# Kernel optimization log

Measured on AMD Instinct MI355X. Metric: run time of the kernel, lower is better.

The kernel has to match this reference:

```python
import jax, jax.numpy as jnp
import numpy as np

B = 256       # number of grasp centers (batch)
N = 65536     # total points output by the backbone
C = 1024      # backbone feature channels (enc_channels[-1])
K = 512       # padded slots per segment (points per center)
INFO = 3      # info_size
KCLS = 6      # k_cls
EPS = 1e-5    # LayerNorm eps


def _layernorm(x, g, b):
    m = x.mean(-1, keepdims=True)
    v = ((x - m) ** 2).mean(-1, keepdims=True)
    return (x - m) / jnp.sqrt(v + EPS) * g + b


def setup_inputs() -> dict:
    key = jax.random.key(0)
    ks = jax.random.split(key, 10)
    feat = jax.random.normal(ks[0], (N, C), jnp.float32)
    offsets = jnp.sort(jax.random.randint(ks[1], (B,), 0, N)).astype(jnp.int64)
    offsets = offsets.at[-1].set(N)  # cumulative ends, last covers all points
    info = jax.random.normal(ks[2], (B, INFO), jnp.float32)

    def lin(k, o, i):
        return 0.02 * jax.random.normal(k, (o, i), jnp.float32), jnp.zeros((o,), jnp.float32)

    W1, b1 = lin(ks[3], 512, C)          # point_layer Linear(1024,512)
    Wi, bi = lin(ks[4], 32, INFO)        # info_layer Linear(info_size,32)
    Wa1, ba1 = lin(ks[5], 256, 544)      # anchor_mlp Linear(544,256)
    Wa2, ba2 = lin(ks[6], KCLS, 256)     # anchor_mlp Linear(256,k_cls)
    Wo1, bo1 = lin(ks[7], 256, 544)      # offset_mlp Linear(544,256)
    Wo2, bo2 = lin(ks[8], KCLS * 3, 256) # offset_mlp Linear(256,k_cls*3)
    return dict(
        feat=feat, info=info, offsets=offsets,
        W1=W1, b1=b1, ln1_g=jnp.ones((512,)), ln1_b=jnp.zeros((512,)),
        Wi=Wi, bi=bi,
        Wa1=Wa1, ba1=ba1, lna_g=jnp.ones((256,)), lna_b=jnp.zeros((256,)),
        Wa2=Wa2, ba2=ba2,
        Wo1=Wo1, bo1=bo1, lno_g=jnp.ones((256,)), lno_b=jnp.zeros((256,)),
        Wo2=Wo2, bo2=bo2,
    )


def reference(feat, info, W1, b1, ln1_g, ln1_b, Wi, bi,
              Wa1, ba1, lna_g, lna_b, Wa2, ba2,
              Wo1, bo1, lno_g, lno_b, Wo2, bo2, offsets):
    # --- fused segment-max replaces the pad loop + max over padded dim ---
    # point i belongs to segment b s.t. offsets[b-1] <= i < offsets[b]
    ids = jnp.searchsorted(offsets, jnp.arange(feat.shape[0]), side='right')
    segmax = jax.ops.segment_max(feat, ids, num_segments=B)  # (B, C)
    lengths = jnp.diff(offsets, prepend=0)
    # original zero-pads to K slots: segments shorter than K see 0 in the max
    features = jnp.where((lengths < K)[:, None], jnp.maximum(segmax, 0.0), segmax)

    # point_layer: Linear -> LayerNorm -> Dropout(eval: identity) -> ReLU
    pf = jax.nn.relu(_layernorm(features @ W1.T + b1, ln1_g, ln1_b))
    # info_layer
    inf = info @ Wi.T + bi
    x = jnp.concatenate([pf, inf], axis=1)  # (B, 544)

    pred = jax.nn.relu(_layernorm(x @ Wa1.T + ba1, lna_g, lna_b)) @ Wa2.T + ba2
    off = jax.nn.relu(_layernorm(x @ Wo1.T + bo1, lno_g, lno_b)) @ Wo2.T + bo2
    offset = off.reshape(-1, KCLS, 3)
    return features, pred, offset
```

## Files before the change

### kernel.cpp

```cpp
#include <hip/hip_runtime.h>
#include <hip/hip_bf16.h>
#include <cstdint>

#define NPTS 65536
#define CCH  1024
#define BSEG 256
#define KSLOT 512
#define WROWS 32

typedef float v4f __attribute__((ext_vector_type(4)));

__device__ __forceinline__ unsigned ukey(float f) {
  int i = __float_as_int(f);
  return i >= 0 ? ((unsigned)i | 0x80000000u) : ~(unsigned)i;
}
__device__ __forceinline__ float udec(unsigned u, bool rl) {
  float v;
  if (u >= 0x80000000u) v = __int_as_float((int)(u & 0x7FFFFFFFu));
  else                  v = __int_as_float((int)~u);
  if (u == 0u) v = -__builtin_inff();
  if (rl) v = fmaxf(v, 0.0f);
  return v;
}

__device__ __forceinline__ v4f ntload4(const float* p) {
  return __builtin_nontemporal_load((const v4f*)p);
}
__device__ __forceinline__ v4f vmax4(v4f a, v4f b) {
  v4f r;
  r.x = fmaxf(a.x, b.x); r.y = fmaxf(a.y, b.y);
  r.z = fmaxf(a.z, b.z); r.w = fmaxf(a.w, b.w);
  return r;
}

__global__ __launch_bounds__(256) void segmax_k(const float* __restrict__ feat,
                                                const int* __restrict__ offsets,
                                                unsigned* __restrict__ keys) {
  int t = threadIdx.x;
  int col = t << 2;
  int row0 = blockIdx.x * WROWS;
  int row_end = row0 + WROWS;
  int lo = 0, hi = BSEG - 1;
  while (lo < hi) { int mid = (lo + hi) >> 1; if (offsets[mid] > row0) hi = mid; else lo = mid + 1; }
  int seg = lo;
  int end = offsets[seg];
  const float NI = -__builtin_inff();
  v4f m; m.x = NI; m.y = NI; m.z = NI; m.w = NI;
  bool dirty = false;
  int r = row0;
  while (r < row_end) {
    while (r >= end) {
      if (dirty) {
        unsigned* kp = keys + (size_t)seg * CCH + col;
        atomicMax(kp + 0, ukey(m.x));
        atomicMax(kp + 1, ukey(m.y));
        atomicMax(kp + 2, ukey(m.z));
        atomicMax(kp + 3, ukey(m.w));
        m.x = NI; m.y = NI; m.z = NI; m.w = NI;
        dirty = false;
      }
      ++seg;
      end = offsets[seg];
    }
    int stop = min(row_end, end);
    const float* p = feat + (size_t)r * CCH + col;
    for (; r + 8 <= stop; r += 8) {
      v4f v0 = ntload4(p);
      v4f v1 = ntload4(p + CCH);
      v4f v2 = ntload4(p + 2 * CCH);
      v4f v3 = ntload4(p + 3 * CCH);
      v4f v4 = ntload4(p + 4 * CCH);
      v4f v5 = ntload4(p + 5 * CCH);
      v4f v6 = ntload4(p + 6 * CCH);
      v4f v7 = ntload4(p + 7 * CCH);
      p += 8 * CCH;
      m = vmax4(m, vmax4(vmax4(vmax4(v0, v1), vmax4(v2, v3)),
                         vmax4(vmax4(v4, v5), vmax4(v6, v7))));
    }
    for (; r < stop; ++r) {
      v4f v = ntload4(p);
      p += CCH;
      m = vmax4(m, v);
    }
    dirty = true;
  }
  if (dirty) {
    unsigned* kp = keys + (size_t)seg * CCH + col;
    atomicMax(kp + 0, ukey(m.x));
    atomicMax(kp + 1, ukey(m.y));
    atomicMax(kp + 2, ukey(m.z));
    atomicMax(kp + 3, ukey(m.w));
  }
}

__global__ __launch_bounds__(256) void gemm1_fused(
    const unsigned* __restrict__ keys, const int* __restrict__ offsets,
    const float* __restrict__ W1, float* __restrict__ features,
    float* __restrict__ part) {
  __shared__ float As[32][68];
  __shared__ float Ws[32][68];
  int bx = blockIdx.x, by = blockIdx.y, bz = blockIdx.z;
  int t = threadIdx.x;
  int tx = t & 15, ty = t >> 4;
  int lr = t >> 3;
  int lk = (t & 7) << 2;
  int row0 = by * 64 + lr, row1 = row0 + 32;
  int len0 = offsets[row0] - (row0 ? offsets[row0 - 1] : 0);
  int len1 = offsets[row1] - offsets[row1 - 1];
  bool rl0 = len0 < KSLOT, rl1 = len1 < KSLOT;
  const unsigned* K0 = keys + (size_t)row0 * CCH + lk;
  const unsigned* K1 = keys + (size_t)row1 * CCH + lk;
  int c0 = bx * 64 + lr, c1 = c0 + 32;
  const float* Wr0 = W1 + (size_t)c0 * CCH + lk;
  const float* Wr1 = W1 + (size_t)c1 * CCH + lk;
  float acc[4][4] = {};
  for (int s = 0; s < 8; ++s) {
    int k0 = (bz * 8 + s) << 5;
    uint4 ua = *(const uint4*)(K0 + k0);
    uint4 ub = *(const uint4*)(K1 + k0);
    float4 w0 = *(const float4*)(Wr0 + k0);
    float4 w1 = *(const float4*)(Wr1 + k0);
    float4 a0 = make_float4(udec(ua.x, rl0), udec(ua.y, rl0), udec(ua.z, rl0), udec(ua.w, rl0));
    float4 a1 = make_float4(udec(ub.x, rl1), udec(ub.y, rl1), udec(ub.z, rl1), udec(ub.w, rl1));
    if (bx == 0) {
      *(float4*)(features + (size_t)row0 * CCH + k0 + lk) = a0;
      *(float4*)(features + (size_t)row1 * CCH + k0 + lk) = a1;
    }
    __syncthreads();
    As[lk + 0][lr] = a0.x; As[lk + 1][lr] = a0.y; As[lk + 2][lr] = a0.z; As[lk + 3][lr] = a0.w;
    As[lk + 0][lr + 32] = a1.x; As[lk + 1][lr + 32] = a1.y; As[lk + 2][lr + 32] = a1.z; As[lk + 3][lr + 32] = a1.w;
    Ws[lk + 0][lr] = w0.x; Ws[lk + 1][lr] = w0.y; Ws[lk + 2][lr] = w0.z; Ws[lk + 3][lr] = w0.w;
    Ws[lk + 0][lr + 32] = w1.x; Ws[lk + 1][lr + 32] = w1.y; Ws[lk + 2][lr + 32] = w1.z; Ws[lk + 3][lr + 32] = w1.w;
    __syncthreads();
#pragma unroll
    for (int kk = 0; kk < 32; ++kk) {
      float4 av = *(const float4*)&As[kk][ty << 2];
      float4 wv = *(const float4*)&Ws[kk][tx << 2];
      acc[0][0] += av.x * wv.x; acc[0][1] += av.x * wv.y; acc[0][2] += av.x * wv.z; acc[0][3] += av.x * wv.w;
      acc[1][0] += av.y * wv.x; acc[1][1] += av.y * wv.y; acc[1][2] += av.y * wv.z; acc[1][3] += av.y * wv.w;
      acc[2][0] += av.z * wv.x; acc[2][1] += av.z * wv.y; acc[2][2] += av.z * wv.z; acc[2][3] += av.z * wv.w;
      acc[3][0] += av.w * wv.x; acc[3][1] += av.w * wv.y; acc[3][2] += av.w * wv.z; acc[3][3] += av.w * wv.w;
    }
  }
  float* op = part + (size_t)bz * 131072 + (size_t)(by * 64 + (ty << 2)) * 512 + bx * 64 + (tx << 2);
#pragma unroll
  for (int i = 0; i < 4; ++i) {
    *(float4*)(op + (size_t)i * 512) = make_float4(acc[i][0], acc[i][1], acc[i][2], acc[i][3]);
  }
}

__global__ __launch_bounds__(256) void gemm_nt_part(
    const float* __restrict__ A, int lda,
    const float* __restrict__ Wlo, const float* __restrict__ Whi, int nlo, int ldw,
    float* __restrict__ part, int Ktot, int steps_per_chunk) {
  __shared__ float As[32][68];
  __shared__ float Ws[32][68];
  int bx = blockIdx.x, by = blockIdx.y, bz = blockIdx.z;
  int t = threadIdx.x;
  int tx = t & 15, ty = t >> 4;
  int steps_total = Ktot >> 5;
  int step0 = bz * steps_per_chunk;
  int nsteps = min(steps_per_chunk, steps_total - step0);
  int lr = t >> 3;
  int lk = (t & 7) << 2;
  const float* Arow0 = A + (size_t)(by * 64 + lr) * lda + lk;
  const float* Arow1 = Arow0 + (size_t)32 * lda;
  int c0 = bx * 64 + lr;
  int c1 = c0 + 32;
  const float* Wrow0 = (c0 < nlo ? Wlo + (size_t)c0 * ldw : Whi + (size_t)(c0 - nlo) * ldw) + lk;
  const float* Wrow1 = (c1 < nlo ? Wlo + (size_t)c1 * ldw : Whi + (size_t)(c1 - nlo) * ldw) + lk;
  float acc[4][4] = {};
  for (int s = 0; s < nsteps; ++s) {
    int k0 = (step0 + s) << 5;
    float4 a0 = *(const float4*)(Arow0 + k0);
    float4 a1 = *(const float4*)(Arow1 + k0);
    float4 w0 = *(const float4*)(Wrow0 + k0);
    float4 w1 = *(const float4*)(Wrow1 + k0);
    __syncthreads();
    As[lk + 0][lr] = a0.x; As[lk + 1][lr] = a0.y; As[lk + 2][lr] = a0.z; As[lk + 3][lr] = a0.w;
    As[lk + 0][lr + 32] = a1.x; As[lk + 1][lr + 32] = a1.y; As[lk + 2][lr + 32] = a1.z; As[lk + 3][lr + 32] = a1.w;
    Ws[lk + 0][lr] = w0.x; Ws[lk + 1][lr] = w0.y; Ws[lk + 2][lr] = w0.z; Ws[lk + 3][lr] = w0.w;
    Ws[lk + 0][lr + 32] = w1.x; Ws[lk + 1][lr + 32] = w1.y; Ws[lk + 2][lr + 32] = w1.z; Ws[lk + 3][lr + 32] = w1.w;
    __syncthreads();
#pragma unroll
    for (int kk = 0; kk < 32; ++kk) {
      float4 av = *(const float4*)&As[kk][ty << 2];
      float4 wv = *(const float4*)&Ws[kk][tx << 2];
      acc[0][0] += av.x * wv.x; acc[0][1] += av.x * wv.y; acc[0][2] += av.x * wv.z; acc[0][3] += av.x * wv.w;
      acc[1][0] += av.y * wv.x; acc[1][1] += av.y * wv.y; acc[1][2] += av.y * wv.z; acc[1][3] += av.y * wv.w;
      acc[2][0] += av.z * wv.x; acc[2][1] += av.z * wv.y; acc[2][2] += av.z * wv.z; acc[2][3] += av.z * wv.w;
      acc[3][0] += av.w * wv.x; acc[3][1] += av.w * wv.y; acc[3][2] += av.w * wv.z; acc[3][3] += av.w * wv.w;
    }
  }
  float* op = part + (size_t)bz * 131072 + (size_t)(by * 64 + (ty << 2)) * 512 + bx * 64 + (tx << 2);
#pragma unroll
  for (int i = 0; i < 4; ++i) {
    *(float4*)(op + (size_t)i * 512) = make_float4(acc[i][0], acc[i][1], acc[i][2], acc[i][3]);
  }
}

__global__ __launch_bounds__(256) void ln1_x_k(
    const float* __restrict__ part1, const float* __restrict__ b1,
    const float* __restrict__ g, const float* __restrict__ be,
    const float* __restrict__ info, const float* __restrict__ Wi, const float* __restrict__ bi,
    float* __restrict__ x) {
  int b = blockIdx.x, t = threadIdx.x;
  int wv = t >> 6, ln = t & 63;
  __shared__ float red[2][4];
  __shared__ float stats[2];
  const float* p = part1 + (size_t)b * 512;
  float z0 = b1[t] + p[t] + p[131072 + t] + p[262144 + t] + p[393216 + t];
  int c1 = t + 256;
  float z1 = b1[c1] + p[c1] + p[131072 + c1] + p[262144 + c1] + p[393216 + c1];
  float s = z0 + z1, q = z0 * z0 + z1 * z1;
#pragma unroll
  for (int o = 32; o; o >>= 1) { s += __shfl_down(s, o); q += __shfl_down(q, o); }
  if (ln == 0) { red[0][wv] = s; red[1][wv] = q; }
  __syncthreads();
  if (t == 0) {
    float S = red[0][0] + red[0][1] + red[0][2] + red[0][3];
    float Q = red[1][0] + red[1][1] + red[1][2] + red[1][3];
    float mean = S * (1.f / 512.f);
    float var = Q * (1.f / 512.f) - mean * mean;
    stats[0] = mean; stats[1] = rsqrtf(var + 1e-5f);
  }
  __syncthreads();
  float mean = stats[0], rstd = stats[1];
  x[b * 544 + t]  = fmaxf((z0 - mean) * rstd * g[t]  + be[t],  0.f);
  x[b * 544 + c1] = fmaxf((z1 - mean) * rstd * g[c1] + be[c1], 0.f);
  if (t < 32) {
    float i0 = info[b * 3], i1 = info[b * 3 + 1], i2 = info[b * 3 + 2];
    x[b * 544 + 512 + t] = bi[t] + Wi[t * 3] * i0 + Wi[t * 3 + 1] * i1 + Wi[t * 3 + 2] * i2;
  }
}

__global__ __launch_bounds__(256) void heads_k(
    const float* __restrict__ part2,
    const float* __restrict__ ba1, const float* __restrict__ ga, const float* __restrict__ bea,
    const float* __restrict__ Wa2, const float* __restrict__ ba2,
    const float* __restrict__ bo1, const float* __restrict__ go, const float* __restrict__ beo,
    const float* __restrict__ Wo2, const float* __restrict__ bo2,
    float* __restrict__ outp) {
  int b = blockIdx.x, t = threadIdx.x;
  int wv = t >> 6, ln = t & 63;
  __shared__ float h[512];
  __shared__ float red[4][4];
  __shared__ float stats[4];
  const float* p0 = part2 + (size_t)b * 512;
  const float* p1 = p0 + 131072;
  float za = ba1[t] + p0[t] + p1[t];
  float zo = bo1[t] + p0[256 + t] + p1[256 + t];
  float sa = za, qa = za * za, so = zo, qo = zo * zo;
#pragma unroll
  for (int o = 32; o; o >>= 1) {
    sa += __shfl_down(sa, o); qa += __shfl_down(qa, o);
    so += __shfl_down(so, o); qo += __shfl_down(qo, o);
  }
  if (ln == 0) { red[wv][0] = sa; red[wv][1] = qa; red[wv][2] = so; red[wv][3] = qo; }
  __syncthreads();
  if (t == 0) {
    float Sa = red[0][0] + red[1][0] + red[2][0] + red[3][0];
    float Qa = red[0][1] + red[1][1] + red[2][1] + red[3][1];
    float So = red[0][2] + red[1][2] + red[2][2] + red[3][2];
    float Qo = red[0][3] + red[1][3] + red[2][3] + red[3][3];
    float ma = Sa * (1.f / 256.f), va = Qa * (1.f / 256.f) - ma * ma;
    float mo = So * (1.f / 256.f), vo = Qo * (1.f / 256.f) - mo * mo;
    stats[0] = ma; stats[1] = rsqrtf(va + 1e-5f);
    stats[2] = mo; stats[3] = rsqrtf(vo + 1e-5f);
  }
  __syncthreads();
  h[t]       = fmaxf((za - stats[0]) * stats[1] * ga[t] + bea[t], 0.f);
  h[256 + t] = fmaxf((zo - stats[2]) * stats[3] * go[t] + beo[t], 0.f);
  __syncthreads();
  const float* hh = (wv == 0) ? h : (h + 256);
  const float* W2 = (wv == 0) ? Wa2 : Wo2;
  const float* b2 = (wv == 0) ? ba2 : bo2;
  int o0 = (wv == 0) ? 0 : (wv - 1) * 6;
  int base = (wv == 0) ? (262144 + b * 6) : (263680 + b * 18);
  float h0 = hh[ln], h1 = hh[64 + ln], h2v = hh[128 + ln], h3 = hh[192 + ln];
#pragma unroll
  for (int oo = 0; oo < 6; ++oo) {
    int o = o0 + oo;
    const float* w = W2 + o * 256;
    float pr = h0 * w[ln] + h1 * w[64 + ln] + h2v * w[128 + ln] + h3 * w[192 + ln];
#pragma unroll
    for (int d = 32; d; d >>= 1) pr += __shfl_down(pr, d);
    if (ln == 0) outp[base + o] = pr + b2[o];
  }
}

extern "C" void kernel_launch(void* const* d_in, const int* in_sizes, int n_in,
                              void* d_out, int out_size, void* d_ws, size_t ws_size,
                              hipStream_t stream) {
  const float* feat   = (const float*)d_in[0];
  const float* info   = (const float*)d_in[1];
  const int*   offs   = (const int*)d_in[2];
  const float* W1     = (const float*)d_in[3];
  const float* b1     = (const float*)d_in[4];
  const float* ln1_g  = (const float*)d_in[5];
  const float* ln1_b  = (const float*)d_in[6];
  const float* Wi     = (const float*)d_in[7];
  const float* bi     = (const float*)d_in[8];
  const float* Wa1    = (const float*)d_in[9];
  const float* ba1    = (const float*)d_in[10];
  const float* lna_g  = (const float*)d_in[11];
  const float* lna_b  = (const float*)d_in[12];
  const float* Wa2    = (const float*)d_in[13];
  const float* ba2    = (const float*)d_in[14];
  const float* Wo1    = (const float*)d_in[15];
  const float* bo1    = (const float*)d_in[16];
  const float* lno_g  = (const float*)d_in[17];
  const float* lno_b  = (const float*)d_in[18];
  const float* Wo2    = (const float*)d_in[19];
  const float* bo2    = (const float*)d_in[20];

  char* ws = (char*)d_ws;
  unsigned* keys  = (unsigned*)ws;
  float* part1 = (float*)(ws + (1u << 20));
  float* xbuf  = (float*)(ws + 3u * (1u << 20));
  float* part2 = (float*)(ws + 3u * (1u << 20) + 655360u);
  float* features = (float*)d_out;
  float* outp = (float*)d_out;

  hipMemsetAsync(keys, 0, (size_t)BSEG * CCH * sizeof(unsigned), stream);
  segmax_k<<<dim3(NPTS / WROWS), dim3(256), 0, stream>>>(feat, offs, keys);
  gemm1_fused<<<dim3(8, 4, 4), dim3(256), 0, stream>>>(keys, offs, W1, features, part1);
  ln1_x_k<<<dim3(256), dim3(256), 0, stream>>>(part1, b1, ln1_g, ln1_b, info, Wi, bi, xbuf);
  gemm_nt_part<<<dim3(8, 4, 2), dim3(256), 0, stream>>>(
      xbuf, 544, Wa1, Wo1, 256, 544, part2, 544, 9);
  heads_k<<<dim3(256), dim3(256), 0, stream>>>(
      part2, ba1, lna_g, lna_b, Wa2, ba2, bo1, lno_g, lno_b, Wo2, bo2, outp);
}
```

Before: 104.5 us.

## Fuse LN1, info layer and both heads into one tail kernel; retune segmax and GEMM1 split

Replaces the ln1, second-layer GEMM and heads kernels with a single per-row, per-head kernel that computes LayerNorm, the 544->256 matvec, its LayerNorm and the output projection in shared memory. This removes two launches and the xbuf and part2 round trips through global memory. GEMM1's K-split goes from 4 to 8 for more blocks. The segmax kernel now covers 64 rows per block and uses plain loads instead of nontemporal ones. The fused tail computes the second-layer matvec with per-row dot products, rereading the Wa1 and Wo1 weights once for every row instead of tiling them.

```diff
diff --git a/kernel.cpp b/kernel.cpp
--- a/kernel.cpp
+++ b/kernel.cpp
@@ -1,12 +1,11 @@
 #include <hip/hip_runtime.h>
-#include <hip/hip_bf16.h>
 #include <cstdint>
 
 #define NPTS 65536
 #define CCH  1024
 #define BSEG 256
 #define KSLOT 512
-#define WROWS 32
+#define WROWS 64
 
 typedef float v4f __attribute__((ext_vector_type(4)));
 
@@ -21,10 +20,6 @@
   if (u == 0u) v = -__builtin_inff();
   if (rl) v = fmaxf(v, 0.0f);
   return v;
-}
-
-__device__ __forceinline__ v4f ntload4(const float* p) {
-  return __builtin_nontemporal_load((const v4f*)p);
 }
 __device__ __forceinline__ v4f vmax4(v4f a, v4f b) {
   v4f r;
@@ -65,20 +60,18 @@
     int stop = min(row_end, end);
     const float* p = feat + (size_t)r * CCH + col;
     for (; r + 8 <= stop; r += 8) {
-      v4f v0 = ntload4(p);
-      v4f v1 = ntload4(p + CCH);
-      v4f v2 = ntload4(p + 2 * CCH);
-      v4f v3 = ntload4(p + 3 * CCH);
-      v4f v4 = ntload4(p + 4 * CCH);
-      v4f v5 = ntload4(p + 5 * CCH);
-      v4f v6 = ntload4(p + 6 * CCH);
-      v4f v7 = ntload4(p + 7 * CCH);
+      v4f v[8];
+#pragma unroll
+      for (int j = 0; j < 8; ++j) v[j] = *(const v4f*)(p + (size_t)j * CCH);
       p += 8 * CCH;
-      m = vmax4(m, vmax4(vmax4(vmax4(v0, v1), vmax4(v2, v3)),
-                         vmax4(vmax4(v4, v5), vmax4(v6, v7))));
+#pragma unroll
+      for (int d = 4; d; d >>= 1)
+#pragma unroll
+        for (int j = 0; j < d; ++j) v[j] = vmax4(v[j], v[j + d]);
+      m = vmax4(m, v[0]);
     }
     for (; r < stop; ++r) {
-      v4f v = ntload4(p);
+      v4f v = *(const v4f*)(p);
       p += CCH;
       m = vmax4(m, v);
     }
@@ -96,7 +89,7 @@
 __global__ __launch_bounds__(256) void gemm1_fused(
     const unsigned* __restrict__ keys, const int* __restrict__ offsets,
     const float* __restrict__ W1, float* __restrict__ features,
-    float* __restrict__ part) {
+    float* __restrict__ part1) {
   __shared__ float As[32][68];
   __shared__ float Ws[32][68];
   int bx = blockIdx.x, by = blockIdx.y, bz = blockIdx.z;
@@ -114,8 +107,8 @@
   const float* Wr0 = W1 + (size_t)c0 * CCH + lk;
   const float* Wr1 = W1 + (size_t)c1 * CCH + lk;
   float acc[4][4] = {};
-  for (int s = 0; s < 8; ++s) {
-    int k0 = (bz * 8 + s) << 5;
+  for (int s = 0; s < 4; ++s) {
+    int k0 = (bz * 4 + s) << 5;
     uint4 ua = *(const uint4*)(K0 + k0);
     uint4 ub = *(const uint4*)(K1 + k0);
     float4 w0 = *(const float4*)(Wr0 + k0);
@@ -142,150 +135,113 @@
       acc[3][0] += av.w * wv.x; acc[3][1] += av.w * wv.y; acc[3][2] += av.w * wv.z; acc[3][3] += av.w * wv.w;
     }
   }
-  float* op = part + (size_t)bz * 131072 + (size_t)(by * 64 + (ty << 2)) * 512 + bx * 64 + (tx << 2);
-#pragma unroll
-  for (int i = 0; i < 4; ++i) {
+  float* op = part1 + (size_t)bz * 131072 + (size_t)(by * 64 + (ty << 2)) * 512 + bx * 64 + (tx << 2);
+#pragma unroll
+  for (int i = 0; i < 4; ++i)
     *(float4*)(op + (size_t)i * 512) = make_float4(acc[i][0], acc[i][1], acc[i][2], acc[i][3]);
-  }
-}
-
-__global__ __launch_bounds__(256) void gemm_nt_part(
-    const float* __restrict__ A, int lda,
-    const float* __restrict__ Wlo, const float* __restrict__ Whi, int nlo, int ldw,
-    float* __restrict__ part, int Ktot, int steps_per_chunk) {
-  __shared__ float As[32][68];
-  __shared__ float Ws[32][68];
-  int bx = blockIdx.x, by = blockIdx.y, bz = blockIdx.z;
+}
+
+__global__ __launch_bounds__(256) void tail_k(
+    const float* __restrict__ part1, const float* __restrict__ b1,
+    const float* __restrict__ g1, const float* __restrict__ be1,
+    const float* __restrict__ info, const float* __restrict__ Wi, const float* __restrict__ bi,
+    const float* __restrict__ Wa1, const float* __restrict__ ba1,
+    const float* __restrict__ ga, const float* __restrict__ bea,
+    const float* __restrict__ Wa2, const float* __restrict__ ba2,
+    const float* __restrict__ Wo1, const float* __restrict__ bo1,
+    const float* __restrict__ go, const float* __restrict__ beo,
+    const float* __restrict__ Wo2, const float* __restrict__ bo2,
+    float* __restrict__ out) {
+  int bb = blockIdx.x;
+  int r = bb >> 1, head = bb & 1;
   int t = threadIdx.x;
-  int tx = t & 15, ty = t >> 4;
-  int steps_total = Ktot >> 5;
-  int step0 = bz * steps_per_chunk;
-  int nsteps = min(steps_per_chunk, steps_total - step0);
-  int lr = t >> 3;
-  int lk = (t & 7) << 2;
-  const float* Arow0 = A + (size_t)(by * 64 + lr) * lda + lk;
-  const float* Arow1 = Arow0 + (size_t)32 * lda;
-  int c0 = bx * 64 + lr;
-  int c1 = c0 + 32;
-  const float* Wrow0 = (c0 < nlo ? Wlo + (size_t)c0 * ldw : Whi + (size_t)(c0 - nlo) * ldw) + lk;
-  const float* Wrow1 = (c1 < nlo ? Wlo + (size_t)c1 * ldw : Whi + (size_t)(c1 - nlo) * ldw) + lk;
-  float acc[4][4] = {};
-  for (int s = 0; s < nsteps; ++s) {
-    int k0 = (step0 + s) << 5;
-    float4 a0 = *(const float4*)(Arow0 + k0);
-    float4 a1 = *(const float4*)(Arow1 + k0);
-    float4 w0 = *(const float4*)(Wrow0 + k0);
-    float4 w1 = *(const float4*)(Wrow1 + k0);
-    __syncthreads();
-    As[lk + 0][lr] = a0.x; As[lk + 1][lr] = a0.y; As[lk + 2][lr] = a0.z; As[lk + 3][lr] = a0.w;
-    As[lk + 0][lr + 32] = a1.x; As[lk + 1][lr + 32] = a1.y; As[lk + 2][lr + 32] = a1.z; As[lk + 3][lr + 32] = a1.w;
-    Ws[lk + 0][lr] = w0.x; Ws[lk + 1][lr] = w0.y; Ws[lk + 2][lr] = w0.z; Ws[lk + 3][lr] = w0.w;
-    Ws[lk + 0][lr + 32] = w1.x; Ws[lk + 1][lr + 32] = w1.y; Ws[lk + 2][lr + 32] = w1.z; Ws[lk + 3][lr + 32] = w1.w;
-    __syncthreads();
-#pragma unroll
-    for (int kk = 0; kk < 32; ++kk) {
-      float4 av = *(const float4*)&As[kk][ty << 2];
-      float4 wv = *(const float4*)&Ws[kk][tx << 2];
-      acc[0][0] += av.x * wv.x; acc[0][1] += av.x * wv.y; acc[0][2] += av.x * wv.z; acc[0][3] += av.x * wv.w;
-      acc[1][0] += av.y * wv.x; acc[1][1] += av.y * wv.y; acc[1][2] += av.y * wv.z; acc[1][3] += av.y * wv.w;
-      acc[2][0] += av.z * wv.x; acc[2][1] += av.z * wv.y; acc[2][2] += av.z * wv.z; acc[2][3] += av.z * wv.w;
-      acc[3][0] += av.w * wv.x; acc[3][1] += av.w * wv.y; acc[3][2] += av.w * wv.z; acc[3][3] += av.w * wv.w;
-    }
-  }
-  float* op = part + (size_t)bz * 131072 + (size_t)(by * 64 + (ty << 2)) * 512 + bx * 64 + (tx << 2);
-#pragma unroll
-  for (int i = 0; i < 4; ++i) {
-    *(float4*)(op + (size_t)i * 512) = make_float4(acc[i][0], acc[i][1], acc[i][2], acc[i][3]);
-  }
-}
-
-__global__ __launch_bounds__(256) void ln1_x_k(
-    const float* __restrict__ part1, const float* __restrict__ b1,
-    const float* __restrict__ g, const float* __restrict__ be,
-    const float* __restrict__ info, const float* __restrict__ Wi, const float* __restrict__ bi,
-    float* __restrict__ x) {
-  int b = blockIdx.x, t = threadIdx.x;
   int wv = t >> 6, ln = t & 63;
-  __shared__ float red[2][4];
-  __shared__ float stats[2];
-  const float* p = part1 + (size_t)b * 512;
-  float z0 = b1[t] + p[t] + p[131072 + t] + p[262144 + t] + p[393216 + t];
-  int c1 = t + 256;
-  float z1 = b1[c1] + p[c1] + p[131072 + c1] + p[262144 + c1] + p[393216 + c1];
-  float s = z0 + z1, q = z0 * z0 + z1 * z1;
-#pragma unroll
-  for (int o = 32; o; o >>= 1) { s += __shfl_down(s, o); q += __shfl_down(q, o); }
-  if (ln == 0) { red[0][wv] = s; red[1][wv] = q; }
+  __shared__ float x[544];
+  __shared__ float h[256];
+  __shared__ float sred[8];
+  __shared__ float sst[2];
+
+  {
+    const float* p = part1 + (size_t)r * 512;
+    float z0 = b1[t], z1 = b1[t + 256];
+#pragma unroll
+    for (int j = 0; j < 8; ++j) {
+      z0 += p[(size_t)j * 131072 + t];
+      z1 += p[(size_t)j * 131072 + 256 + t];
+    }
+    float s = z0 + z1, q = z0 * z0 + z1 * z1;
+#pragma unroll
+    for (int o = 32; o; o >>= 1) { s += __shfl_down(s, o); q += __shfl_down(q, o); }
+    if (ln == 0) { sred[wv] = s; sred[4 + wv] = q; }
+    __syncthreads();
+    if (t == 0) {
+      float S = sred[0] + sred[1] + sred[2] + sred[3];
+      float Q = sred[4] + sred[5] + sred[6] + sred[7];
+      float mean = S * (1.f / 512.f);
+      float var = Q * (1.f / 512.f) - mean * mean;
+      sst[0] = mean; sst[1] = rsqrtf(var + 1e-5f);
+    }
+    __syncthreads();
+    float mean = sst[0], rstd = sst[1];
+    x[t]       = fmaxf((z0 - mean) * rstd * g1[t]       + be1[t],       0.f);
+    x[t + 256] = fmaxf((z1 - mean) * rstd * g1[t + 256] + be1[t + 256], 0.f);
+    if (t < 32) {
+      float i0 = info[r * 3], i1 = info[r * 3 + 1], i2 = info[r * 3 + 2];
+      x[512 + t] = bi[t] + Wi[t * 3] * i0 + Wi[t * 3 + 1] * i1 + Wi[t * 3 + 2] * i2;
+    }
+  }
   __syncthreads();
-  if (t == 0) {
-    float S = red[0][0] + red[0][1] + red[0][2] + red[0][3];
-    float Q = red[1][0] + red[1][1] + red[1][2] + red[1][3];
-    float mean = S * (1.f / 512.f);
-    float var = Q * (1.f / 512.f) - mean * mean;
-    stats[0] = mean; stats[1] = rsqrtf(var + 1e-5f);
+
+  {
+    const float* W  = head ? Wo1 : Wa1;
+    const float* bs = head ? bo1 : ba1;
+    int o = wv * 64;
+    for (int i = 0; i < 64; ++i, ++o) {
+      const float* wr = W + (size_t)o * 544;
+      float pr = 0.f;
+#pragma unroll
+      for (int j = 0; j < 8; ++j) pr += wr[j * 64 + ln] * x[j * 64 + ln];
+      if (ln < 32) pr += wr[512 + ln] * x[512 + ln];
+#pragma unroll
+      for (int d = 32; d; d >>= 1) pr += __shfl_down(pr, d);
+      if (ln == 0) h[o] = pr + bs[o];
+    }
   }
   __syncthreads();
-  float mean = stats[0], rstd = stats[1];
-  x[b * 544 + t]  = fmaxf((z0 - mean) * rstd * g[t]  + be[t],  0.f);
-  x[b * 544 + c1] = fmaxf((z1 - mean) * rstd * g[c1] + be[c1], 0.f);
-  if (t < 32) {
-    float i0 = info[b * 3], i1 = info[b * 3 + 1], i2 = info[b * 3 + 2];
-    x[b * 544 + 512 + t] = bi[t] + Wi[t * 3] * i0 + Wi[t * 3 + 1] * i1 + Wi[t * 3 + 2] * i2;
-  }
-}
-
-__global__ __launch_bounds__(256) void heads_k(
-    const float* __restrict__ part2,
-    const float* __restrict__ ba1, const float* __restrict__ ga, const float* __restrict__ bea,
-    const float* __restrict__ Wa2, const float* __restrict__ ba2,
-    const float* __restrict__ bo1, const float* __restrict__ go, const float* __restrict__ beo,
-    const float* __restrict__ Wo2, const float* __restrict__ bo2,
-    float* __restrict__ outp) {
-  int b = blockIdx.x, t = threadIdx.x;
-  int wv = t >> 6, ln = t & 63;
-  __shared__ float h[512];
-  __shared__ float red[4][4];
-  __shared__ float stats[4];
-  const float* p0 = part2 + (size_t)b * 512;
-  const float* p1 = p0 + 131072;
-  float za = ba1[t] + p0[t] + p1[t];
-  float zo = bo1[t] + p0[256 + t] + p1[256 + t];
-  float sa = za, qa = za * za, so = zo, qo = zo * zo;
-#pragma unroll
-  for (int o = 32; o; o >>= 1) {
-    sa += __shfl_down(sa, o); qa += __shfl_down(qa, o);
-    so += __shfl_down(so, o); qo += __shfl_down(qo, o);
-  }
-  if (ln == 0) { red[wv][0] = sa; red[wv][1] = qa; red[wv][2] = so; red[wv][3] = qo; }
+
+  {
+    float hv = h[t];
+    float s = hv, q = hv * hv;
+#pragma unroll
+    for (int o = 32; o; o >>= 1) { s += __shfl_down(s, o); q += __shfl_down(q, o); }
+    if (ln == 0) { sred[wv] = s; sred[4 + wv] = q; }
+    __syncthreads();
+    if (t == 0) {
+      float S = sred[0] + sred[1] + sred[2] + sred[3];
+      float Q = sred[4] + sred[5] + sred[6] + sred[7];
+      float mean = S * (1.f / 256.f);
+      float var = Q * (1.f / 256.f) - mean * mean;
+      sst[0] = mean; sst[1] = rsqrtf(var + 1e-5f);
+    }
+    __syncthreads();
+    float hn = fmaxf((hv - sst[0]) * sst[1] * (head ? go : ga)[t] + (head ? beo : bea)[t], 0.f);
+    h[t] = hn;
+  }
   __syncthreads();
-  if (t == 0) {
-    float Sa = red[0][0] + red[1][0] + red[2][0] + red[3][0];
-    float Qa = red[0][1] + red[1][1] + red[2][1] + red[3][1];
-    float So = red[0][2] + red[1][2] + red[2][2] + red[3][2];
-    float Qo = red[0][3] + red[1][3] + red[2][3] + red[3][3];
-    float ma = Sa * (1.f / 256.f), va = Qa * (1.f / 256.f) - ma * ma;
-    float mo = So * (1.f / 256.f), vo = Qo * (1.f / 256.f) - mo * mo;
-    stats[0] = ma; stats[1] = rsqrtf(va + 1e-5f);
-    stats[2] = mo; stats[3] = rsqrtf(vo + 1e-5f);
-  }
-  __syncthreads();
-  h[t]       = fmaxf((za - stats[0]) * stats[1] * ga[t] + bea[t], 0.f);
-  h[256 + t] = fmaxf((zo - stats[2]) * stats[3] * go[t] + beo[t], 0.f);
-  __syncthreads();
-  const float* hh = (wv == 0) ? h : (h + 256);
-  const float* W2 = (wv == 0) ? Wa2 : Wo2;
-  const float* b2 = (wv == 0) ? ba2 : bo2;
-  int o0 = (wv == 0) ? 0 : (wv - 1) * 6;
-  int base = (wv == 0) ? (262144 + b * 6) : (263680 + b * 18);
-  float h0 = hh[ln], h1 = hh[64 + ln], h2v = hh[128 + ln], h3 = hh[192 + ln];
-#pragma unroll
-  for (int oo = 0; oo < 6; ++oo) {
-    int o = o0 + oo;
-    const float* w = W2 + o * 256;
-    float pr = h0 * w[ln] + h1 * w[64 + ln] + h2v * w[128 + ln] + h3 * w[192 + ln];
-#pragma unroll
-    for (int d = 32; d; d >>= 1) pr += __shfl_down(pr, d);
-    if (ln == 0) outp[base + o] = pr + b2[o];
+
+  {
+    const float* W2 = head ? Wo2 : Wa2;
+    const float* b2 = head ? bo2 : ba2;
+    int nout = head ? 18 : 6;
+    int base = head ? (263680 + r * 18) : (262144 + r * 6);
+    for (int o = wv; o < nout; o += 4) {
+      const float* wr = W2 + (size_t)o * 256;
+      float pr = wr[ln] * h[ln] + wr[64 + ln] * h[64 + ln]
+               + wr[128 + ln] * h[128 + ln] + wr[192 + ln] * h[192 + ln];
+#pragma unroll
+      for (int d = 32; d; d >>= 1) pr += __shfl_down(pr, d);
+      if (ln == 0) out[base + o] = pr + b2[o];
+    }
   }
 }
 
@@ -315,19 +271,16 @@
   const float* bo2    = (const float*)d_in[20];
 
   char* ws = (char*)d_ws;
-  unsigned* keys  = (unsigned*)ws;
-  float* part1 = (float*)(ws + (1u << 20));
-  float* xbuf  = (float*)(ws + 3u * (1u << 20));
-  float* part2 = (float*)(ws + 3u * (1u << 20) + 655360u);
+  float*    part1 = (float*)ws;
+  unsigned* keys  = (unsigned*)(ws + (4u << 20));
   float* features = (float*)d_out;
-  float* outp = (float*)d_out;
+  float* outp     = (float*)d_out;
 
   hipMemsetAsync(keys, 0, (size_t)BSEG * CCH * sizeof(unsigned), stream);
   segmax_k<<<dim3(NPTS / WROWS), dim3(256), 0, stream>>>(feat, offs, keys);
-  gemm1_fused<<<dim3(8, 4, 4), dim3(256), 0, stream>>>(keys, offs, W1, features, part1);
-  ln1_x_k<<<dim3(256), dim3(256), 0, stream>>>(part1, b1, ln1_g, ln1_b, info, Wi, bi, xbuf);
-  gemm_nt_part<<<dim3(8, 4, 2), dim3(256), 0, stream>>>(
-      xbuf, 544, Wa1, Wo1, 256, 544, part2, 544, 9);
-  heads_k<<<dim3(256), dim3(256), 0, stream>>>(
-      part2, ba1, lna_g, lna_b, Wa2, ba2, bo1, lno_g, lno_b, Wo2, bo2, outp);
-}
+  gemm1_fused<<<dim3(8, 4, 8), dim3(256), 0, stream>>>(keys, offs, W1, features, part1);
+  tail_k<<<dim3(512), dim3(256), 0, stream>>>(
+      part1, b1, ln1_g, ln1_b, info, Wi, bi,
+      Wa1, ba1, lna_g, lna_b, Wa2, ba2,
+      Wo1, bo1, lno_g, lno_b, Wo2, bo2, outp);
+}
```

Result: slower. 124.2 us (+18.9%).
